# Optimization experiments

Hardware: AMD Instinct MI355X
Metric: run time of the kernel (lower is better)

The kernel has to match this reference:

```python
import jax, jax.numpy as jnp
import numpy as np

# ---- config (matches init_kwargs + VMamba/MambaIR SS2D defaults) ----
B, LEN, C, H, W = 2, 3, 64, 64, 64
N_STATE = 16           # d_state
D_INNER = 2 * C        # expand=2
DT_RANK = C // 16      # ceil(d_model/16)
K = 4                  # 4 scan directions
EPS = 1e-5


def _ln_last(x, g, b):
    m = x.mean(-1, keepdims=True)
    v = x.var(-1, keepdims=True)
    return (x - m) * jax.lax.rsqrt(v + EPS) * g + b


def _instance_ln(x):
    # kalman.utils.layer_norm: normalize each sample over (C,H,W), no affine
    m = x.mean(axis=(1, 2, 3), keepdims=True)
    v = x.var(axis=(1, 2, 3), keepdims=True)
    return (x - m) * jax.lax.rsqrt(v + EPS)


def _gn(x, g, b):
    # GroupNorm with num_groups=1 on NCHW
    m = x.mean(axis=(1, 2, 3), keepdims=True)
    v = x.var(axis=(1, 2, 3), keepdims=True)
    return (x - m) * jax.lax.rsqrt(v + EPS) * g[None, :, None, None] + b[None, :, None, None]


def _conv2d(x, w, b, groups=1):
    y = jax.lax.conv_general_dilated(x, w, (1, 1), 'SAME',
            dimension_numbers=('NCHW', 'OIHW', 'NCHW'), feature_group_count=groups)
    return y + b[None, :, None, None]


def _selective_scan(xs, dts, Bs, Cs, A, Ds, dt_bias):
    # xs, dts: (Bt,K,D,L); Bs, Cs: (Bt,K,N,L); A: (K,D,N); Ds, dt_bias: (K,D)
    delta = jax.nn.softplus(dts + dt_bias[None, :, :, None])
    u_t = jnp.moveaxis(xs, -1, 0)      # (L,Bt,K,D)
    d_t = jnp.moveaxis(delta, -1, 0)
    B_t = jnp.moveaxis(Bs, -1, 0)      # (L,Bt,K,N)
    C_t = jnp.moveaxis(Cs, -1, 0)
    h0 = jnp.zeros((xs.shape[0], K, xs.shape[2], A.shape[-1]), xs.dtype)

    def step(h, inp):
        u, d, Bv, Cv = inp
        dA = jnp.exp(d[..., None] * A)                                  # (Bt,K,D,N)
        h = dA * h + d[..., None] * Bv[:, :, None, :] * u[..., None]
        y = jnp.einsum('bkdn,bkn->bkd', h, Cv)
        return h, y

    _, ys = jax.lax.scan(step, h0, (u_t, d_t, B_t, C_t))
    ys = jnp.moveaxis(ys, 0, -1)                                        # (Bt,K,D,L)
    return ys + xs * Ds[None, :, :, None]


def _ss2d(x, in_proj_w, dwconv_w, dwconv_b, x_proj_w, dt_proj_w, dt_proj_b,
          A_logs, Ds, out_norm_g, out_norm_b, out_proj_w):
    Bt, Hh, Ww, Cc = x.shape
    L = Hh * Ww
    xz = x @ in_proj_w.T                               # (Bt,H,W,2*Di)
    xx, z = jnp.split(xz, 2, axis=-1)
    xx = jnp.transpose(xx, (0, 3, 1, 2))               # (Bt,Di,H,W)
    xx = jax.nn.silu(_conv2d(xx, dwconv_w, dwconv_b, groups=D_INNER))
    hw = xx.reshape(Bt, D_INNER, L)
    wh = jnp.transpose(xx, (0, 1, 3, 2)).reshape(Bt, D_INNER, L)
    xs = jnp.stack([hw, wh, hw[..., ::-1], wh[..., ::-1]], axis=1)      # (Bt,4,Di,L)
    x_dbl = jnp.einsum('bkdl,kcd->bkcl', xs, x_proj_w)
    dts = jnp.einsum('bkrl,kdr->bkdl', x_dbl[:, :, :DT_RANK], dt_proj_w)
    Bs = x_dbl[:, :, DT_RANK:DT_RANK + N_STATE]
    Cs = x_dbl[:, :, DT_RANK + N_STATE:]
    A = -jnp.exp(A_logs)                               # (K,Di,N)
    out_y = _selective_scan(xs, dts, Bs, Cs, A, Ds, dt_proj_b)
    inv = out_y[:, 2:4, :, ::-1]

    def wh2hw(y):
        return jnp.transpose(y.reshape(Bt, D_INNER, Ww, Hh), (0, 1, 3, 2)).reshape(Bt, D_INNER, L)

    y = out_y[:, 0] + inv[:, 0] + wh2hw(out_y[:, 1]) + wh2hw(inv[:, 1])
    y = jnp.transpose(y.reshape(Bt, D_INNER, Hh, Ww), (0, 2, 3, 1))
    y = _ln_last(y, out_norm_g, out_norm_b)
    y = y * jax.nn.silu(z)
    return y @ out_proj_w.T


def setup_inputs() -> dict:
    key = jax.random.key(0)
    ks = jax.random.split(key, 16)
    rn = lambda k, s, sc=0.05: jax.random.normal(k, s, jnp.float32) * sc
    inp = {}
    inp['image_sequence'] = jax.random.normal(ks[0], (B, LEN, C, H, W), jnp.float32)
    inp['difficult_zone'] = jax.random.normal(ks[1], (B, C, H, W), jnp.float32)
    inp['sigma'] = jax.random.uniform(ks[2], (B, C, H, W), jnp.float32)
    inp['gn1_g'] = jnp.ones((3 * C,)); inp['gn1_b'] = jnp.zeros((3 * C,))
    inp['conv1_w'] = rn(ks[3], (C, 3 * C, 3, 3)); inp['conv1_b'] = jnp.zeros((C,))
    inp['gn2_g'] = jnp.ones((C,)); inp['gn2_b'] = jnp.zeros((C,))
    inp['conv2_w'] = rn(ks[4], (C, C, 3, 3)); inp['conv2_b'] = jnp.zeros((C,))
    inp['skip_w'] = rn(ks[5], (C, 3 * C, 1, 1)); inp['skip_b'] = jnp.zeros((C,))
    inp['ln1_g'] = jnp.ones((C,)); inp['ln1_b'] = jnp.zeros((C,))
    inp['ln2_g'] = jnp.ones((C,)); inp['ln2_b'] = jnp.zeros((C,))
    inp['in_proj_w'] = rn(ks[6], (2 * D_INNER, C))
    inp['dwconv_w'] = rn(ks[7], (D_INNER, 1, 3, 3)); inp['dwconv_b'] = jnp.zeros((D_INNER,))
    inp['x_proj_w'] = rn(ks[8], (K, DT_RANK + 2 * N_STATE, D_INNER))
    inp['dt_proj_w'] = rn(ks[9], (K, D_INNER, DT_RANK), 0.2)
    inp['dt_proj_b'] = rn(ks[10], (K, D_INNER), 0.1)
    inp['A_logs'] = jnp.log(jnp.broadcast_to(jnp.arange(1, N_STATE + 1, dtype=jnp.float32), (K, D_INNER, N_STATE)))
    inp['Ds'] = jnp.ones((K, D_INNER))
    inp['out_norm_g'] = jnp.ones((D_INNER,)); inp['out_norm_b'] = jnp.zeros((D_INNER,))
    inp['out_proj_w'] = rn(ks[11], (C, D_INNER))
    inp['fc1_w'] = rn(ks[12], (C, C)); inp['fc1_b'] = jnp.zeros((C,))
    inp['fc2_w'] = rn(ks[13], (C, C)); inp['fc2_b'] = jnp.zeros((C,))
    return inp


def reference(image_sequence, difficult_zone, sigma,
              gn1_g, gn1_b, conv1_w, conv1_b, gn2_g, gn2_b, conv2_w, conv2_b, skip_w, skip_b,
              ln1_g, ln1_b, ln2_g, ln2_b,
              in_proj_w, dwconv_w, dwconv_b, x_proj_w, dt_proj_w, dt_proj_b,
              A_logs, Ds, out_norm_g, out_norm_b, out_proj_w,
              fc1_w, fc1_b, fc2_w, fc2_b):
    Bsz, Lf, Cc, Hh, Ww = image_sequence.shape
    # per-frame layer_norm; frames are independent so fold them into batch
    img = _instance_ln(image_sequence.reshape(Bsz * Lf, Cc, Hh, Ww)).reshape(Bsz, Lf, Cc, Hh, Ww)
    dz = jnp.broadcast_to(difficult_zone[:, None], (Bsz, Lf, Cc, Hh, Ww))
    sg = jnp.broadcast_to(sigma[:, None], (Bsz, Lf, Cc, Hh, Ww))
    x = jnp.concatenate([dz, img, sg], axis=2).reshape(Bsz * Lf, 3 * Cc, Hh, Ww)
    # ConvolutionalResBlock (GN -> SiLU -> conv, x2, + 1x1 skip)
    h = _conv2d(jax.nn.silu(_gn(x, gn1_g, gn1_b)), conv1_w, conv1_b)
    h = _conv2d(jax.nn.silu(_gn(h, gn2_g, gn2_b)), conv2_w, conv2_b)
    x = h + _conv2d(x, skip_w, skip_b)
    # VSSBlock (pre-norm): x + SS2D(LN(x)); x + Mlp(LN(x))
    x = jnp.transpose(x, (0, 2, 3, 1))                 # NHWC
    x = x + _ss2d(_ln_last(x, ln1_g, ln1_b), in_proj_w, dwconv_w, dwconv_b,
                  x_proj_w, dt_proj_w, dt_proj_b, A_logs, Ds,
                  out_norm_g, out_norm_b, out_proj_w)
    xm = _ln_last(x, ln2_g, ln2_b)
    x = x + (jax.nn.gelu(xm @ fc1_w.T + fc1_b) @ fc2_w.T + fc2_b)
    x = jnp.transpose(x, (0, 3, 1, 2)).reshape(Bsz, Lf, Cc, Hh, Ww)
    return x
```

## Files before the change

kernel.cpp:

```cpp
#include <hip/hip_runtime.h>
#include <hip/hip_bf16.h>

typedef unsigned short ushortT;
typedef short short8v __attribute__((ext_vector_type(8)));
typedef float float4v __attribute__((ext_vector_type(4)));

#define NBL 6
#define NC 64
#define NC3 192
#define NHW 4096
#define NDI 128
#define NNS 16
#define NDR 4
#define NK 4
#define NL 4096
#define NCH 128
#define SCLEN 32
#define NSTATE 49152

static const size_t F_XCAT  = 0;
static const size_t F_ACT1  = 4718592;
static const size_t F_H1    = 9437184;
static const size_t F_ACT2  = 11010048;
static const size_t F_H2    = 12582912;
static const size_t F_XRES  = 14155776;
static const size_t F_XXIN  = 15728640;
static const size_t F_Z     = 18874368;
static const size_t F_XXC   = 22020096;
static const size_t F_XDBL  = 25165824;
static const size_t F_YS    = 28704768;
static const size_t F_X1    = 44433408;
static const size_t F_X2    = 46006272;
static const size_t F_STATS = 47579136;
static const size_t F_TOTAL = 47579184;

__device__ __forceinline__ float wred64(float v) {
#pragma unroll
  for (int m = 32; m; m >>= 1) v += __shfl_xor(v, m, 64);
  return v;
}

__device__ __forceinline__ float silu(float v) {
  return v / (1.f + __expf(-v));
}

__device__ __forceinline__ ushortT f2bf(float f) {
  unsigned int u = __builtin_bit_cast(unsigned int, f);
  unsigned int r = (u + 0x7FFFu + ((u >> 16) & 1u)) >> 16;
  return (ushortT)r;
}

__device__ __forceinline__ float bf2f(ushortT u) {
  return __builtin_bit_cast(float, (unsigned int)u << 16);
}

__device__ __forceinline__ int map_pos(int k, int l) {
  if (k == 0) return l;
  if (k == 1) return ((l & 63) << 6) | (l >> 6);
  if (k == 2) return 4095 - l;
  int lp = 4095 - l;
  return ((lp & 63) << 6) | (lp >> 6);
}

__device__ __forceinline__ float softplus_fast(float a) {
  float t = exp2f(a * 1.44269504f);
  float r = 0.69314718f * __log2f(1.f + t);
  return (a > 20.f) ? a : r;
}

__device__ __forceinline__ void pow_tree(float E1, float4v& e0, float4v& e1,
                                         float4v& e2, float4v& e3) {
  float E2 = E1 * E1, E3 = E2 * E1, E4 = E2 * E2;
  float E5 = E4 * E1, E6 = E4 * E2, E7 = E4 * E3, E8 = E4 * E4;
  e0[0] = E1; e0[1] = E2; e0[2] = E3; e0[3] = E4;
  e1[0] = E5; e1[1] = E6; e1[2] = E7; e1[3] = E8;
  e2[0] = E8 * E1; e2[1] = E8 * E2; e2[2] = E8 * E3; e2[3] = E8 * E4;
  e3[0] = E8 * E5; e3[1] = E8 * E6; e3[2] = E8 * E7; e3[3] = E8 * E8;
}

__global__ __launch_bounds__(256) void wtrans_kernel(const float* __restrict__ src,
                                                     float* __restrict__ dst, int O, int C) {
  int id = blockIdx.x * 256 + threadIdx.x;
  if (id >= O * C) return;
  int c = id / O, o = id % O;
  dst[id] = src[o * C + c];
}

__global__ __launch_bounds__(256) void stats1_kernel(const float* __restrict__ in, int n,
                                                     double* __restrict__ part) {
  int bi = blockIdx.x;
  int s = bi >> 5, j = bi & 31;
  int slice = n >> 5;
  const float4* p = (const float4*)(in + (size_t)s * n + (size_t)j * slice);
  int n4 = slice >> 2;
  double dsum = 0.0, dsq = 0.0;
  for (int i = threadIdx.x; i < n4; i += 256) {
    float4 v = p[i];
    dsum += (double)((v.x + v.y) + (v.z + v.w));
    dsq += (double)v.x * v.x + (double)v.y * v.y + (double)v.z * v.z + (double)v.w * v.w;
  }
  __shared__ double s1[256], s2[256];
  s1[threadIdx.x] = dsum; s2[threadIdx.x] = dsq;
  __syncthreads();
  for (int off = 128; off; off >>= 1) {
    if (threadIdx.x < off) { s1[threadIdx.x] += s1[threadIdx.x + off]; s2[threadIdx.x] += s2[threadIdx.x + off]; }
    __syncthreads();
  }
  if (threadIdx.x == 0) { part[2 * bi] = s1[0]; part[2 * bi + 1] = s2[0]; }
}

__global__ __launch_bounds__(64) void stats2_kernel(const double* __restrict__ part, int n,
                                                    float* __restrict__ mean_out,
                                                    float* __restrict__ rstd_out) {
  int s = blockIdx.x;
  int lane = threadIdx.x;
  double sum = 0.0, sq = 0.0;
  if (lane < 32) { sum = part[2 * (s * 32 + lane)]; sq = part[2 * (s * 32 + lane) + 1]; }
#pragma unroll
  for (int m = 16; m; m >>= 1) { sum += __shfl_xor(sum, m, 64); sq += __shfl_xor(sq, m, 64); }
  if (lane == 0) {
    double mean = sum / n;
    double var = sq / n - mean * mean;
    mean_out[s] = (float)mean;
    rstd_out[s] = (float)(1.0 / sqrt(var + 1e-5));
  }
}

__global__ __launch_bounds__(256) void build_xcat_kernel(const float* __restrict__ img,
                                                         const float* __restrict__ dz,
                                                         const float* __restrict__ sg,
                                                         const float* __restrict__ stats,
                                                         float* __restrict__ xcat) {
  size_t gid = (size_t)blockIdx.x * 256 + threadIdx.x;
  int p = gid & 4095;
  size_t r = gid >> 12;
  int ch = (int)(r % NC3);
  int bl = (int)(r / NC3);
  int b = bl / 3;
  float v;
  if (ch < 64) {
    v = dz[((size_t)b * NC + ch) * NHW + p];
  } else if (ch < 128) {
    float m = stats[bl], rs = stats[8 + bl];
    v = (img[((size_t)bl * NC + (ch - 64)) * NHW + p] - m) * rs;
  } else {
    v = sg[((size_t)b * NC + (ch - 128)) * NHW + p];
  }
  xcat[gid] = v;
}

template <int CCH>
__global__ __launch_bounds__(256) void gnsilu_t_kernel(const float* __restrict__ in,
                                                       const float* __restrict__ g,
                                                       const float* __restrict__ b,
                                                       const float* __restrict__ stats,
                                                       ushortT* __restrict__ outb) {
  int bi = blockIdx.x;
  int bl = bi >> 6, h = bi & 63;
  __shared__ ushortT tile[CCH][66];
  float m = stats[bl], rs = stats[8 + bl];
  int t = threadIdx.x;
  for (int idx = t; idx < CCH * 64; idx += 256) {
    int ch = idx >> 6, w = idx & 63;
    float v = in[(((size_t)bl * CCH + ch) << 12) + (h << 6) + w];
    v = (v - m) * rs * g[ch] + b[ch];
    v = silu(v);
    tile[ch][w] = f2bf(v);
  }
  __syncthreads();
  constexpr int C8 = CCH / 8;
  for (int idx = t; idx < 64 * C8; idx += 256) {
    int w = idx / C8, c8 = idx % C8;
    short8v v;
#pragma unroll
    for (int j = 0; j < 8; ++j) v[j] = (short)tile[c8 * 8 + j][w];
    *(short8v*)&outb[(size_t)(bl * 4096 + h * 64 + w) * CCH + c8 * 8] = v;
  }
}

__global__ __launch_bounds__(256) void wprep_kernel(const float* __restrict__ w,
                                                    ushortT* __restrict__ out,
                                                    int CIN, int KT) {
  int id = blockIdx.x * 256 + threadIdx.x;
  int j = id & 7;
  int lane = (id >> 3) & 63;
  int nt = (id >> 9) & 3;
  int rest = id >> 11;
  int kt = rest % KT;
  int tap = rest / KT;
  int oc = nt * 16 + (lane & 15);
  int ic = kt * 32 + ((lane >> 4) << 3) + j;
  int r = tap / 3, s = tap % 3;
  out[id] = f2bf(w[(((size_t)oc * CIN + ic) * 3 + r) * 3 + s]);
}

template <int CIN>
__global__ __launch_bounds__(256) void conv_mfma_kernel(const ushortT* __restrict__ actb,
                                                        const ushortT* __restrict__ wb,
                                                        const float* __restrict__ bias,
                                                        float* __restrict__ out) {
  constexpr int KT = CIN / 32;
  constexpr int STRIDE = CIN + 8;
  constexpr int C8 = CIN / 8;
  int bi = blockIdx.x;
  int nh = bi & 1;
  int h = (bi >> 1) & 63;
  int bl = bi >> 7;
  int t = threadIdx.x;
  int wv = t >> 6, lane = t & 63;
  __shared__ ushortT lds[66 * STRIDE];
  float4v acc0 = {0.f, 0.f, 0.f, 0.f};
  float4v acc1 = {0.f, 0.f, 0.f, 0.f};
  int lrow = lane & 15;
  int lk = (lane >> 4) << 3;
  for (int dy = 0; dy < 3; ++dy) {
    int hh = h + dy - 1;
    bool valid = (hh >= 0) && (hh < 64);
    int hc = valid ? hh : 0;
    if (dy) __syncthreads();
    const ushortT* src = actb + (size_t)(bl * 4096 + hc * 64) * CIN;
    for (int idx = t; idx < 64 * C8; idx += 256) {
      int w = idx / C8, c8 = idx % C8;
      short8v v = {0, 0, 0, 0, 0, 0, 0, 0};
      if (valid) v = *(const short8v*)&src[(size_t)w * CIN + c8 * 8];
      *(short8v*)&lds[(w + 1) * STRIDE + c8 * 8] = v;
    }
    if (t < 2 * C8) {
      int which = t / C8, c8 = t % C8;
      short8v z = {0, 0, 0, 0, 0, 0, 0, 0};
      *(short8v*)&lds[(which ? 65 : 0) * STRIDE + c8 * 8] = z;
    }
    __syncthreads();
    for (int dx = 0; dx < 3; ++dx) {
      int tap = dy * 3 + dx;
      int wl = (wv << 4) + lrow + dx;
#pragma unroll
      for (int kt = 0; kt < KT; ++kt) {
        short8v a = *(const short8v*)&lds[wl * STRIDE + kt * 32 + lk];
        const ushortT* wp = wb + ((size_t)(((tap * KT + kt) * 4 + (nh << 1)) * 64 + lane) << 3);
        short8v b0 = *(const short8v*)&wp[0];
        short8v b1 = *(const short8v*)&wp[512];
        acc0 = __builtin_amdgcn_mfma_f32_16x16x32_bf16(a, b0, acc0, 0, 0, 0);
        acc1 = __builtin_amdgcn_mfma_f32_16x16x32_bf16(a, b1, acc1, 0, 0, 0);
      }
    }
  }
  int oc0 = (nh << 5) + lrow;
  int oc1 = oc0 + 16;
  int w0 = (wv << 4) + ((lane >> 4) << 2);
  float bv0 = bias[oc0], bv1 = bias[oc1];
  float4 o0 = make_float4(acc0[0] + bv0, acc0[1] + bv0, acc0[2] + bv0, acc0[3] + bv0);
  float4 o1 = make_float4(acc1[0] + bv1, acc1[1] + bv1, acc1[2] + bv1, acc1[3] + bv1);
  *(float4*)&out[(((size_t)bl * 64 + oc0) << 12) + (h << 6) + w0] = o0;
  *(float4*)&out[(((size_t)bl * 64 + oc1) << 12) + (h << 6) + w0] = o1;
}

__global__ __launch_bounds__(256) void skip_kernel(const float* __restrict__ xcat,
                                                   const float* __restrict__ h2,
                                                   const float* __restrict__ skwt,
                                                   const float* __restrict__ skb,
                                                   float* __restrict__ xres) {
  int bi = blockIdx.x;
  int bl = bi >> 6, h = bi & 63;
  int t = threadIdx.x;
  int oc = t & 63, w0 = (t >> 6) << 4;
  __shared__ float lds[64][64];
  float acc[16];
#pragma unroll
  for (int i = 0; i < 16; ++i) acc[i] = 0.f;
  for (int cc = 0; cc < 3; ++cc) {
    __syncthreads();
    for (int idx = t; idx < 4096; idx += 256) {
      int ch = idx >> 6, w = idx & 63;
      lds[ch][w] = xcat[(((size_t)bl * NC3 + cc * 64 + ch) << 12) + (h << 6) + w];
    }
    __syncthreads();
    for (int ch = 0; ch < 64; ++ch) {
      float wv = skwt[((cc << 6) + ch) * 64 + oc];
#pragma unroll
      for (int i = 0; i < 16; ++i) acc[i] += wv * lds[ch][w0 + i];
    }
  }
  float bv = skb[oc];
  int p0 = (h << 6) + w0;
#pragma unroll
  for (int i = 0; i < 16; ++i) {
    float hv = h2[(((size_t)bl * 64 + oc) << 12) + p0 + i];
    xres[((size_t)bl * NHW + p0 + i) * 64 + oc] = acc[i] + bv + hv;
  }
}

__global__ __launch_bounds__(256) void inproj_kernel(const float* __restrict__ xres,
                                                     const float* __restrict__ g,
                                                     const float* __restrict__ b,
                                                     const float* __restrict__ wt,
                                                     float* __restrict__ xxin,
                                                     float* __restrict__ z) {
  int wv = threadIdx.x >> 6, lane = threadIdx.x & 63;
  size_t pi0 = (size_t)blockIdx.x << 4;
  __shared__ float xb[64][16];
  float gv = g[lane], bv = b[lane];
#pragma unroll
  for (int j = 0; j < 4; ++j) {
    int p = (wv << 2) + j;
    float x = xres[(pi0 + p) * 64 + lane];
    float s = wred64(x);
    float s2 = wred64(x * x);
    float m = s * (1.f / 64), var = s2 * (1.f / 64) - m * m;
    float rstd = rsqrtf(var + 1e-5f);
    xb[lane][p] = (x - m) * rstd * gv + bv;
  }
  __syncthreads();
  int oc = (wv << 6) + lane;
  float4v a0 = {0.f, 0.f, 0.f, 0.f}, a1 = a0, a2 = a0, a3 = a0;
  for (int c = 0; c < 64; ++c) {
    float w = wt[(c << 8) + oc];
    const float4v* xr = (const float4v*)&xb[c][0];
    a0 += w * xr[0];
    a1 += w * xr[1];
    a2 += w * xr[2];
    a3 += w * xr[3];
  }
  float acc[16];
  *(float4v*)&acc[0] = a0;
  *(float4v*)&acc[4] = a1;
  *(float4v*)&acc[8] = a2;
  *(float4v*)&acc[12] = a3;
  float* dst = (oc < 128) ? xxin : z;
  int oco = (oc < 128) ? oc : (oc - 128);
#pragma unroll
  for (int p = 0; p < 16; ++p) dst[((pi0 + p) << 7) + oco] = acc[p];
}

__global__ __launch_bounds__(256) void dwconv_kernel(const float* __restrict__ xx,
                                                     const float* __restrict__ w,
                                                     const float* __restrict__ b,
                                                     float* __restrict__ out) {
  size_t gid = (size_t)blockIdx.x * 256 + threadIdx.x;
  int d = gid & 127;
  size_t pi = gid >> 7;
  int p = (int)(pi & 4095);
  int bl = (int)(pi >> 12);
  int h = p >> 6, wq = p & 63;
  float acc = b[d];
  const float* wr = w + d * 9;
#pragma unroll
  for (int dy = -1; dy <= 1; ++dy) {
    int hh = h + dy;
    if (hh < 0 || hh >= 64) continue;
#pragma unroll
    for (int dx = -1; dx <= 1; ++dx) {
      int ww = wq + dx;
      if (ww < 0 || ww >= 64) continue;
      acc += wr[(dy + 1) * 3 + (dx + 1)] * xx[(((size_t)bl << 12) + (hh << 6) + ww) * 128 + d];
    }
  }
  out[pi * 128 + d] = silu(acc);
}

__global__ __launch_bounds__(256) void xdbl_kernel(const float* __restrict__ xxc,
                                                   const float* __restrict__ xpw,
                                                   float* __restrict__ xdbl) {
  int bi = blockIdx.x;
  int lt = bi & 63;
  int korder = (bi >> 6) & 1;
  int bl = bi >> 7;
  int lbase = lt << 6;
  __shared__ float xs[64 * 128];
  int t = threadIdx.x;
#pragma unroll
  for (int it = 0; it < 8; ++it) {
    int idx = it * 256 + t;
    int i = idx >> 5, d4 = idx & 31;
    int l = lbase + i;
    int pos = korder ? (((l & 63) << 6) | (l >> 6)) : l;
    float4 v = *(const float4*)&xxc[((size_t)bl * NHW + pos) * 128 + (d4 << 2)];
    int slot = d4 ^ (i & 7);
    *(float4*)&xs[i * 128 + (slot << 2)] = v;
  }
  __syncthreads();
  int wv = __builtin_amdgcn_readfirstlane(t >> 6);
  int lane = t & 63;
  int k_w = korder + ((wv >= 2) ? 2 : 0);
  int c0 = (wv & 1) * 18;
  float acc[18];
#pragma unroll
  for (int j = 0; j < 18; ++j) acc[j] = 0.f;
  const float* wbase = xpw + (size_t)(k_w * 36 + c0) * 128;
  for (int d4 = 0; d4 < 32; ++d4) {
    int slot = d4 ^ (lane & 7);
    float4 x4 = *(const float4*)&xs[lane * 128 + (slot << 2)];
#pragma unroll
    for (int j = 0; j < 18; ++j) {
      float4 w4 = *(const float4*)&wbase[j * 128 + (d4 << 2)];
      acc[j] += w4.x * x4.x + w4.y * x4.y + w4.z * x4.z + w4.w * x4.w;
    }
  }
  int lout = (k_w < 2) ? (lbase + lane) : (4095 - lbase - lane);
  size_t obase = ((size_t)(bl * 4 + k_w) * 36 + c0) * (size_t)NL + lout;
#pragma unroll
  for (int j = 0; j < 18; ++j)
    xdbl[obase + (size_t)j * NL] = acc[j];
}

__global__ __launch_bounds__(128) void scan_pass1_kernel(const float* __restrict__ xdbl,
                                                         const float* __restrict__ xxc,
                                                         const float* __restrict__ dtw,
                                                         const float* __restrict__ dtb,
                                                         const float* __restrict__ Alog,
                                                         float* __restrict__ chunkSdt,
                                                         ushortT* __restrict__ chunkH16) {
  int bi = blockIdx.x;
  int chunk = bi & (NCH - 1);
  int bk = bi >> 7;
  int k = bk & 3, bl = bk >> 2;
  int d = threadIdx.x;
  float4 wv = *(const float4*)(dtw + (size_t)(((k << 7) + d) << 2));
  float bias = dtb[(k << 7) + d];
  const float* ar = Alog + (size_t)(((k << 7) + d) << 4);
  float a1v = -__expf(ar[0]) * 1.44269504f;
  bool geom = true;
#pragma unroll
  for (int n = 1; n < 16; ++n) {
    float an = -__expf(ar[n]) * 1.44269504f;
    geom = geom && (fabsf(an - (float)(n + 1) * a1v) <= 1e-3f * fabsf((float)(n + 1) * a1v) + 1e-6f);
  }
  __shared__ float xd[SCLEN][20];
  int l0 = chunk << 5;
  for (int idx = threadIdx.x; idx < 20 * SCLEN; idx += 128) {
    int c = idx >> 5, li = idx & 31;
    xd[li][c] = xdbl[((size_t)bk * 36 + c) * (size_t)NL + l0 + li];
  }
  __syncthreads();
  const float* uB = xxc + ((size_t)bl << 19) + d;
  float4v h0 = {0.f, 0.f, 0.f, 0.f}, h1 = h0, h2 = h0, h3 = h0;
  float sdt = 0.f;
  float u_nxt = uB[(size_t)map_pos(k, l0) << 7];
  if (geom) {
    for (int li = 0; li < SCLEN; ++li) {
      float u = u_nxt;
      int nl = (li < SCLEN - 1) ? (li + 1) : (SCLEN - 1);
      u_nxt = uB[(size_t)map_pos(k, l0 + nl) << 7];
      const float4v* row = (const float4v*)&xd[li][0];
      float4v q0 = row[0];
      float accq = bias + wv.x * q0[0] + wv.y * q0[1] + wv.z * q0[2] + wv.w * q0[3];
      float dt = softplus_fast(accq);
      float dtu = dt * u;
      sdt += dt;
      float4v b0 = row[1], b1 = row[2], b2 = row[3], b3 = row[4];
      float4v e0, e1, e2, e3;
      pow_tree(exp2f(a1v * dt), e0, e1, e2, e3);
      h0 = e0 * h0 + dtu * b0;
      h1 = e1 * h1 + dtu * b1;
      h2 = e2 * h2 + dtu * b2;
      h3 = e3 * h3 + dtu * b3;
    }
  } else {
    float4v a0v, a1q, a2q, a3q;
#pragma unroll
    for (int j = 0; j < 4; ++j) {
      a0v[j] = -__expf(ar[j]) * 1.44269504f;
      a1q[j] = -__expf(ar[4 + j]) * 1.44269504f;
      a2q[j] = -__expf(ar[8 + j]) * 1.44269504f;
      a3q[j] = -__expf(ar[12 + j]) * 1.44269504f;
    }
    for (int li = 0; li < SCLEN; ++li) {
      float u = u_nxt;
      int nl = (li < SCLEN - 1) ? (li + 1) : (SCLEN - 1);
      u_nxt = uB[(size_t)map_pos(k, l0 + nl) << 7];
      const float4v* row = (const float4v*)&xd[li][0];
      float4v q0 = row[0];
      float accq = bias + wv.x * q0[0] + wv.y * q0[1] + wv.z * q0[2] + wv.w * q0[3];
      float dt = softplus_fast(accq);
      float dtu = dt * u;
      sdt += dt;
      float4v b0 = row[1], b1 = row[2], b2 = row[3], b3 = row[4];
      float4v e0, e1, e2, e3;
#pragma unroll
      for (int j = 0; j < 4; ++j) {
        e0[j] = exp2f(a0v[j] * dt);
        e1[j] = exp2f(a1q[j] * dt);
        e2[j] = exp2f(a2q[j] * dt);
        e3[j] = exp2f(a3q[j] * dt);
      }
      h0 = e0 * h0 + dtu * b0;
      h1 = e1 * h1 + dtu * b1;
      h2 = e2 * h2 + dtu * b2;
      h3 = e3 * h3 + dtu * b3;
    }
  }
  size_t base = (size_t)chunk * NSTATE + (((size_t)bk << 7) + (size_t)d) * 16;
  chunkSdt[(size_t)chunk * 3072 + (bk << 7) + d] = sdt;
  short8v s0, s1;
#pragma unroll
  for (int j = 0; j < 4; ++j) {
    s0[j] = (short)f2bf(h0[j]);
    s0[4 + j] = (short)f2bf(h1[j]);
    s1[j] = (short)f2bf(h2[j]);
    s1[4 + j] = (short)f2bf(h3[j]);
  }
  *(short8v*)&chunkH16[base + 0] = s0;
  *(short8v*)&chunkH16[base + 8] = s1;
}

__global__ __launch_bounds__(256) void scan_pass2_kernel(const float* __restrict__ chunkSdt,
                                                         const ushortT* __restrict__ chunkH16,
                                                         const float* __restrict__ Alog,
                                                         ushortT* __restrict__ chunkHS16) {
  size_t state = (size_t)blockIdx.x * 256 + threadIdx.x;
  float an = -__expf(Alog[state & 8191]) * 1.44269504f;
  int kd = (int)(state >> 4);
  float h = 0.f;
  for (int j = 0; j < NCH; ++j) {
    size_t idx = (size_t)j * NSTATE + state;
    chunkHS16[idx] = f2bf(h);
    float sdt = chunkSdt[(size_t)j * 3072 + kd];
    h = exp2f(an * sdt) * h + bf2f(chunkH16[idx]);
  }
}

__global__ __launch_bounds__(128) void scan_pass3_kernel(const float* __restrict__ xdbl,
                                                         const float* __restrict__ xxc,
                                                         const float* __restrict__ dtw,
                                                         const float* __restrict__ dtb,
                                                         const float* __restrict__ Alog,
                                                         const ushortT* __restrict__ chunkHS16,
                                                         ushortT* __restrict__ ys16) {
  int bi = blockIdx.x;
  int chunk = bi & (NCH - 1);
  int bk = bi >> 7;
  int k = bk & 3, bl = bk >> 2;
  int d = threadIdx.x;
  float4 wv = *(const float4*)(dtw + (size_t)(((k << 7) + d) << 2));
  float bias = dtb[(k << 7) + d];
  const float* ar = Alog + (size_t)(((k << 7) + d) << 4);
  float a1v = -__expf(ar[0]) * 1.44269504f;
  bool geom = true;
#pragma unroll
  for (int n = 1; n < 16; ++n) {
    float an = -__expf(ar[n]) * 1.44269504f;
    geom = geom && (fabsf(an - (float)(n + 1) * a1v) <= 1e-3f * fabsf((float)(n + 1) * a1v) + 1e-6f);
  }
  __shared__ float xd[SCLEN][36];
  int l0 = chunk << 5;
  for (int idx = threadIdx.x; idx < 36 * SCLEN; idx += 128) {
    int c = idx >> 5, li = idx & 31;
    xd[li][c] = xdbl[((size_t)bk * 36 + c) * (size_t)NL + l0 + li];
  }
  __syncthreads();
  const float* uB = xxc + ((size_t)bl << 19) + d;
  ushortT* yB = ys16 + ((size_t)bk << 19) + d;
  size_t base = (size_t)chunk * NSTATE + (((size_t)bk << 7) + (size_t)d) * 16;
  float4v h0, h1, h2, h3;
  {
    short8v s0 = *(const short8v*)&chunkHS16[base + 0];
    short8v s1 = *(const short8v*)&chunkHS16[base + 8];
#pragma unroll
    for (int j = 0; j < 4; ++j) {
      h0[j] = bf2f((ushortT)s0[j]);
      h1[j] = bf2f((ushortT)s0[4 + j]);
      h2[j] = bf2f((ushortT)s1[j]);
      h3[j] = bf2f((ushortT)s1[4 + j]);
    }
  }
  float u_nxt = uB[(size_t)map_pos(k, l0) << 7];
  if (geom) {
    for (int li = 0; li < SCLEN; ++li) {
      float u = u_nxt;
      int nl = (li < SCLEN - 1) ? (li + 1) : (SCLEN - 1);
      u_nxt = uB[(size_t)map_pos(k, l0 + nl) << 7];
      const float4v* row = (const float4v*)&xd[li][0];
      float4v q0 = row[0];
      float accq = bias + wv.x * q0[0] + wv.y * q0[1] + wv.z * q0[2] + wv.w * q0[3];
      float dt = softplus_fast(accq);
      float dtu = dt * u;
      float4v b0 = row[1], b1 = row[2], b2 = row[3], b3 = row[4];
      float4v c0 = row[5], c1 = row[6], c2 = row[7], c3 = row[8];
      float4v e0, e1, e2, e3;
      pow_tree(exp2f(a1v * dt), e0, e1, e2, e3);
      h0 = e0 * h0 + dtu * b0;
      h1 = e1 * h1 + dtu * b1;
      h2 = e2 * h2 + dtu * b2;
      h3 = e3 * h3 + dtu * b3;
      float4v sy = h0 * c0;
      sy += h1 * c1;
      sy += h2 * c2;
      sy += h3 * c3;
      yB[(size_t)(l0 + li) << 7] = f2bf((sy[0] + sy[1]) + (sy[2] + sy[3]));
    }
  } else {
    float4v a0v, a1q, a2q, a3q;
#pragma unroll
    for (int j = 0; j < 4; ++j) {
      a0v[j] = -__expf(ar[j]) * 1.44269504f;
      a1q[j] = -__expf(ar[4 + j]) * 1.44269504f;
      a2q[j] = -__expf(ar[8 + j]) * 1.44269504f;
      a3q[j] = -__expf(ar[12 + j]) * 1.44269504f;
    }
    for (int li = 0; li < SCLEN; ++li) {
      float u = u_nxt;
      int nl = (li < SCLEN - 1) ? (li + 1) : (SCLEN - 1);
      u_nxt = uB[(size_t)map_pos(k, l0 + nl) << 7];
      const float4v* row = (const float4v*)&xd[li][0];
      float4v q0 = row[0];
      float accq = bias + wv.x * q0[0] + wv.y * q0[1] + wv.z * q0[2] + wv.w * q0[3];
      float dt = softplus_fast(accq);
      float dtu = dt * u;
      float4v b0 = row[1], b1 = row[2], b2 = row[3], b3 = row[4];
      float4v c0 = row[5], c1 = row[6], c2 = row[7], c3 = row[8];
      float4v e0, e1, e2, e3;
#pragma unroll
      for (int j = 0; j < 4; ++j) {
        e0[j] = exp2f(a0v[j] * dt);
        e1[j] = exp2f(a1q[j] * dt);
        e2[j] = exp2f(a2q[j] * dt);
        e3[j] = exp2f(a3q[j] * dt);
      }
      h0 = e0 * h0 + dtu * b0;
      h1 = e1 * h1 + dtu * b1;
      h2 = e2 * h2 + dtu * b2;
      h3 = e3 * h3 + dtu * b3;
      float4v sy = h0 * c0;
      sy += h1 * c1;
      sy += h2 * c2;
      sy += h3 * c3;
      yB[(size_t)(l0 + li) << 7] = f2bf((sy[0] + sy[1]) + (sy[2] + sy[3]));
    }
  }
}

__global__ __launch_bounds__(256) void outproj_kernel(const ushortT* __restrict__ ys16,
                                                      const float* __restrict__ xxc,
                                                      const float* __restrict__ Ds,
                                                      const float* __restrict__ z,
                                                      const float* __restrict__ ong,
                                                      const float* __restrict__ onb,
                                                      const float* __restrict__ opwt,
                                                      const float* __restrict__ xres,
                                                      float* __restrict__ x1) {
  int wv = threadIdx.x >> 6, lane = threadIdx.x & 63;
  size_t pi0 = (size_t)blockIdx.x << 4;
  __shared__ float gb[128][16];
  float og0 = ong[lane], ob0 = onb[lane];
  float og1 = ong[64 + lane], ob1 = onb[64 + lane];
  float ds0 = Ds[lane] + Ds[128 + lane] + Ds[256 + lane] + Ds[384 + lane];
  float ds1 = Ds[64 + lane] + Ds[192 + lane] + Ds[320 + lane] + Ds[448 + lane];
#pragma unroll
  for (int j = 0; j < 4; ++j) {
    int p = (wv << 2) + j;
    size_t pp = pi0 + p;
    int bl = (int)(pp >> 12);
    int pg = (int)(pp & 4095);
    int h = pg >> 6, w = pg & 63;
    int l1 = (w << 6) | h;
    size_t base = ((size_t)bl * 4) << 12;
    size_t i0 = (base + pg) << 7;
    size_t i1 = (base + 4096 + l1) << 7;
    size_t i2 = (base + 2 * 4096 + (4095 - pg)) << 7;
    size_t i3 = (base + 3 * 4096 + (4095 - l1)) << 7;
    float xx0 = xxc[(pp << 7) + lane], xx1 = xxc[(pp << 7) + 64 + lane];
    float y0 = bf2f(ys16[i0 + lane]) + bf2f(ys16[i1 + lane]) + bf2f(ys16[i2 + lane]) +
               bf2f(ys16[i3 + lane]) + xx0 * ds0;
    float y1 = bf2f(ys16[i0 + 64 + lane]) + bf2f(ys16[i1 + 64 + lane]) +
               bf2f(ys16[i2 + 64 + lane]) + bf2f(ys16[i3 + 64 + lane]) + xx1 * ds1;
    float s = wred64(y0 + y1);
    float s2 = wred64(y0 * y0 + y1 * y1);
    float m = s * (1.f / 128), var = s2 * (1.f / 128) - m * m;
    float rstd = rsqrtf(var + 1e-5f);
    float z0 = z[(pp << 7) + lane], z1 = z[(pp << 7) + 64 + lane];
    gb[lane][p] = ((y0 - m) * rstd * og0 + ob0) * silu(z0);
    gb[64 + lane][p] = ((y1 - m) * rstd * og1 + ob1) * silu(z1);
  }
  __syncthreads();
  int p0 = wv << 2;
  float4v acc = {0.f, 0.f, 0.f, 0.f};
  for (int c = 0; c < 128; ++c) {
    float w = opwt[(c << 6) + lane];
    acc += w * (*(const float4v*)&gb[c][p0]);
  }
  float accs[4];
  *(float4v*)&accs[0] = acc;
#pragma unroll
  for (int j = 0; j < 4; ++j) {
    size_t pp = pi0 + p0 + j;
    x1[pp * 64 + lane] = xres[pp * 64 + lane] + accs[j];
  }
}

__global__ __launch_bounds__(256) void mlp_kernel(const float* __restrict__ x1,
                                                  const float* __restrict__ g2,
                                                  const float* __restrict__ b2,
                                                  const float* __restrict__ w1t,
                                                  const float* __restrict__ bb1,
                                                  const float* __restrict__ w2t,
                                                  const float* __restrict__ bb2,
                                                  float* __restrict__ out) {
  int wv = threadIdx.x >> 6, lane = threadIdx.x & 63;
  size_t pi0 = (size_t)blockIdx.x << 4;
  __shared__ float xb[64][16], tb[64][16];
  __shared__ float ot[64][17];
  float gv = g2[lane], bv = b2[lane];
  float xsave[4];
#pragma unroll
  for (int j = 0; j < 4; ++j) {
    int p = (wv << 2) + j;
    float xv = x1[(pi0 + p) * 64 + lane];
    xsave[j] = xv;
    float s = wred64(xv), s2 = wred64(xv * xv);
    float m = s * (1.f / 64), var = s2 * (1.f / 64) - m * m;
    float rstd = rsqrtf(var + 1e-5f);
    xb[lane][p] = (xv - m) * rstd * gv + bv;
  }
  __syncthreads();
  int p0 = wv << 2;
  float bb1v = bb1[lane];
  float4v acc = {bb1v, bb1v, bb1v, bb1v};
  for (int c = 0; c < 64; ++c) {
    float w = w1t[(c << 6) + lane];
    acc += w * (*(const float4v*)&xb[c][p0]);
  }
  float us[4];
  *(float4v*)&us[0] = acc;
#pragma unroll
  for (int j = 0; j < 4; ++j) {
    float u = us[j];
    float tt = tanhf(0.7978845608028654f * (u + 0.044715f * u * u * u));
    tb[lane][p0 + j] = 0.5f * u * (1.f + tt);
  }
  __syncthreads();
  float bb2v = bb2[lane];
  float4v acc2 = {bb2v, bb2v, bb2v, bb2v};
  for (int c = 0; c < 64; ++c) {
    float w = w2t[(c << 6) + lane];
    acc2 += w * (*(const float4v*)&tb[c][p0]);
  }
  float o2[4];
  *(float4v*)&o2[0] = acc2;
#pragma unroll
  for (int j = 0; j < 4; ++j)
    ot[lane][p0 + j] = xsave[j] + o2[j];
  __syncthreads();
  int bl = (int)(pi0 >> 12);
  int pg0 = (int)(pi0 & 4095);
  int t = threadIdx.x;
  int c = t >> 2, q = t & 3;
  float4 v = make_float4(ot[c][(q << 2) + 0], ot[c][(q << 2) + 1],
                         ot[c][(q << 2) + 2], ot[c][(q << 2) + 3]);
  *(float4*)&out[(((size_t)bl * 64 + c) << 12) + pg0 + (q << 2)] = v;
}

extern "C" void kernel_launch(void* const* d_in, const int* in_sizes, int n_in,
                              void* d_out, int out_size, void* d_ws, size_t ws_size,
                              hipStream_t stream) {
  const float* img  = (const float*)d_in[0];
  const float* dz   = (const float*)d_in[1];
  const float* sg   = (const float*)d_in[2];
  const float* gn1g = (const float*)d_in[3];
  const float* gn1b = (const float*)d_in[4];
  const float* c1w  = (const float*)d_in[5];
  const float* c1b  = (const float*)d_in[6];
  const float* gn2g = (const float*)d_in[7];
  const float* gn2b = (const float*)d_in[8];
  const float* c2w  = (const float*)d_in[9];
  const float* c2b  = (const float*)d_in[10];
  const float* skw  = (const float*)d_in[11];
  const float* skb  = (const float*)d_in[12];
  const float* ln1g = (const float*)d_in[13];
  const float* ln1b = (const float*)d_in[14];
  const float* ln2g = (const float*)d_in[15];
  const float* ln2b = (const float*)d_in[16];
  const float* ipw  = (const float*)d_in[17];
  const float* dww  = (const float*)d_in[18];
  const float* dwb  = (const float*)d_in[19];
  const float* xpw  = (const float*)d_in[20];
  const float* dtw  = (const float*)d_in[21];
  const float* dtb  = (const float*)d_in[22];
  const float* Alog = (const float*)d_in[23];
  const float* Dsp  = (const float*)d_in[24];
  const float* ong  = (const float*)d_in[25];
  const float* onb  = (const float*)d_in[26];
  const float* opw  = (const float*)d_in[27];
  const float* f1w  = (const float*)d_in[28];
  const float* f1b  = (const float*)d_in[29];
  const float* f2w  = (const float*)d_in[30];
  const float* f2b  = (const float*)d_in[31];

  float* out = (float*)d_out;
  float* ws = (float*)d_ws;
  if (ws_size < F_TOTAL * sizeof(float)) return;

  float* xcat  = ws + F_XCAT;
  float* h1    = ws + F_H1;
  float* h2    = ws + F_H2;
  float* xres  = ws + F_XRES;
  float* xxin  = ws + F_XXIN;
  float* zbuf  = ws + F_Z;
  float* xxc   = ws + F_XXC;
  float* xdbl  = ws + F_XDBL;
  float* x1    = ws + F_X1;
  float* stats = ws + F_STATS;
  ushortT* act1b = (ushortT*)(ws + F_ACT1);
  ushortT* act2b = (ushortT*)(ws + F_ACT2);
  double* part  = (double*)(ws + F_X2);
  ushortT* wb1  = (ushortT*)(ws + F_X2 + 1024);
  ushortT* wb2  = wb1 + 110592;
  ushortT* ys16     = (ushortT*)(ws + F_YS);
  ushortT* chunkH16 = (ushortT*)(ws + F_YS + 6291456);
  float*   chunkSdt = ws + F_YS + 6291456 + 3145728;
  ushortT* chunkHS16 = (ushortT*)(ws + F_XCAT);
  float* wt_sk = ws + F_ACT1;
  float* wt_ip = ws + F_XCAT;
  float* wt_op = ws + F_XXIN;
  float* wt_f1 = ws + F_XXIN + 8192;
  float* wt_f2 = ws + F_XXIN + 12288;

  wprep_kernel<<<432, 256, 0, stream>>>(c1w, wb1, NC3, 6);
  wprep_kernel<<<144, 256, 0, stream>>>(c2w, wb2, NC, 2);
  stats1_kernel<<<NBL * 32, 256, 0, stream>>>(img, NC * NHW, part);
  stats2_kernel<<<NBL, 64, 0, stream>>>(part, NC * NHW, stats + 0, stats + 8);
  build_xcat_kernel<<<18432, 256, 0, stream>>>(img, dz, sg, stats, xcat);
  stats1_kernel<<<NBL * 32, 256, 0, stream>>>(xcat, NC3 * NHW, part);
  stats2_kernel<<<NBL, 64, 0, stream>>>(part, NC3 * NHW, stats + 16, stats + 24);
  gnsilu_t_kernel<NC3><<<NBL * 64, 256, 0, stream>>>(xcat, gn1g, gn1b, stats + 16, act1b);
  conv_mfma_kernel<NC3><<<NBL * 64 * 2, 256, 0, stream>>>(act1b, wb1, c1b, h1);
  wtrans_kernel<<<48, 256, 0, stream>>>(skw, wt_sk, 64, 192);
  stats1_kernel<<<NBL * 32, 256, 0, stream>>>(h1, NC * NHW, part);
  stats2_kernel<<<NBL, 64, 0, stream>>>(part, NC * NHW, stats + 32, stats + 40);
  gnsilu_t_kernel<NC><<<NBL * 64, 256, 0, stream>>>(h1, gn2g, gn2b, stats + 32, act2b);
  conv_mfma_kernel<NC><<<NBL * 64 * 2, 256, 0, stream>>>(act2b, wb2, c2b, h2);
  skip_kernel<<<NBL * 64, 256, 0, stream>>>(xcat, h2, wt_sk, skb, xres);
  wtrans_kernel<<<64, 256, 0, stream>>>(ipw, wt_ip, 256, 64);
  inproj_kernel<<<1536, 256, 0, stream>>>(xres, ln1g, ln1b, wt_ip, xxin, zbuf);
  dwconv_kernel<<<12288, 256, 0, stream>>>(xxin, dww, dwb, xxc);
  wtrans_kernel<<<32, 256, 0, stream>>>(opw, wt_op, 64, 128);
  wtrans_kernel<<<16, 256, 0, stream>>>(f1w, wt_f1, 64, 64);
  wtrans_kernel<<<16, 256, 0, stream>>>(f2w, wt_f2, 64, 64);
  xdbl_kernel<<<NBL * 2 * 64, 256, 0, stream>>>(xxc, xpw, xdbl);
  scan_pass1_kernel<<<24 * NCH, 128, 0, stream>>>(xdbl, xxc, dtw, dtb, Alog, chunkSdt, chunkH16);
  scan_pass2_kernel<<<192, 256, 0, stream>>>(chunkSdt, chunkH16, Alog, chunkHS16);
  scan_pass3_kernel<<<24 * NCH, 128, 0, stream>>>(xdbl, xxc, dtw, dtb, Alog, chunkHS16, ys16);
  outproj_kernel<<<1536, 256, 0, stream>>>(ys16, xxc, Dsp, zbuf, ong, onb, wt_op, xres, x1);
  mlp_kernel<<<1536, 256, 0, stream>>>(x1, ln2g, ln2b, wt_f1, f1b, wt_f2, f2b, out);
}
```

Before: 343.9 us.

## Eliminate xcat buffer by computing GN1 stats analytically and fusing concat into consumers

Folds all weight transposes and conv weight prep into one prep kernel. Computes the GroupNorm statistics of the concatenated input analytically from per-source sums, using the instance-normalized image's known variance, so the concatenated tensor is never materialized. The GN+SiLU and skip kernels now read dz/img/sg directly. This removes a large write and re-read of xcat plus several launches. It also adds unroll pragmas in the scan loops and pads a shared-memory tile.

```diff
diff --git a/kernel.cpp b/kernel.cpp
--- a/kernel.cpp
+++ b/kernel.cpp
@@ -17,6 +17,7 @@
 #define NCH 128
 #define SCLEN 32
 #define NSTATE 49152
+#define NSAMP 262144
 
 static const size_t F_XCAT  = 0;
 static const size_t F_ACT1  = 4718592;
@@ -29,6 +30,7 @@
 static const size_t F_XXC   = 22020096;
 static const size_t F_XDBL  = 25165824;
 static const size_t F_YS    = 28704768;
+static const size_t F_WTS   = 41287680;
 static const size_t F_X1    = 44433408;
 static const size_t F_X2    = 46006272;
 static const size_t F_STATS = 47579136;
@@ -78,12 +80,89 @@
   e3[0] = E8 * E5; e3[1] = E8 * E6; e3[2] = E8 * E7; e3[3] = E8 * E8;
 }
 
-__global__ __launch_bounds__(256) void wtrans_kernel(const float* __restrict__ src,
-                                                     float* __restrict__ dst, int O, int C) {
-  int id = blockIdx.x * 256 + threadIdx.x;
-  if (id >= O * C) return;
-  int c = id / O, o = id % O;
-  dst[id] = src[o * C + c];
+__global__ __launch_bounds__(256) void prep_kernel(const float* __restrict__ skw,
+                                                   const float* __restrict__ ipw,
+                                                   const float* __restrict__ opw,
+                                                   const float* __restrict__ f1w,
+                                                   const float* __restrict__ f2w,
+                                                   const float* __restrict__ c1w,
+                                                   const float* __restrict__ c2w,
+                                                   float* __restrict__ wt_sk,
+                                                   float* __restrict__ wt_ip,
+                                                   float* __restrict__ wt_op,
+                                                   float* __restrict__ wt_f1,
+                                                   float* __restrict__ wt_f2,
+                                                   ushortT* __restrict__ wb1,
+                                                   ushortT* __restrict__ wb2) {
+  int bi = blockIdx.x;
+  int t = threadIdx.x;
+  if (bi < 48) {
+    int id = bi * 256 + t;
+    int c = id / 64, o = id % 64;
+    wt_sk[id] = skw[o * 192 + c];
+  } else if (bi < 112) {
+    int id = (bi - 48) * 256 + t;
+    int c = id / 256, o = id % 256;
+    wt_ip[id] = ipw[o * 64 + c];
+  } else if (bi < 144) {
+    int id = (bi - 112) * 256 + t;
+    int c = id / 64, o = id % 64;
+    wt_op[id] = opw[o * 128 + c];
+  } else if (bi < 160) {
+    int id = (bi - 144) * 256 + t;
+    int c = id / 64, o = id % 64;
+    wt_f1[id] = f1w[o * 64 + c];
+  } else if (bi < 176) {
+    int id = (bi - 160) * 256 + t;
+    int c = id / 64, o = id % 64;
+    wt_f2[id] = f2w[o * 64 + c];
+  } else if (bi < 608) {
+    int id = (bi - 176) * 256 + t;
+    int j = id & 7, lane = (id >> 3) & 63, nt = (id >> 9) & 3;
+    int rest = id >> 11;
+    int kt = rest % 6, tap = rest / 6;
+    int oc = nt * 16 + (lane & 15);
+    int ic = kt * 32 + ((lane >> 4) << 3) + j;
+    int r = tap / 3, s = tap % 3;
+    wb1[id] = f2bf(c1w[(((size_t)oc * 192 + ic) * 3 + r) * 3 + s]);
+  } else {
+    int id = (bi - 608) * 256 + t;
+    int j = id & 7, lane = (id >> 3) & 63, nt = (id >> 9) & 3;
+    int rest = id >> 11;
+    int kt = rest % 2, tap = rest / 2;
+    int oc = nt * 16 + (lane & 15);
+    int ic = kt * 32 + ((lane >> 4) << 3) + j;
+    int r = tap / 3, s = tap % 3;
+    wb2[id] = f2bf(c2w[(((size_t)oc * 64 + ic) * 3 + r) * 3 + s]);
+  }
+}
+
+__global__ __launch_bounds__(256) void stats1_all_kernel(const float* __restrict__ img,
+                                                         const float* __restrict__ dz,
+                                                         const float* __restrict__ sg,
+                                                         double* __restrict__ part) {
+  int bi = blockIdx.x;
+  int s = bi >> 5, j = bi & 31;
+  const float* srcb = (s < 6) ? (img + (size_t)s * NSAMP)
+                   : (s < 8) ? (dz + (size_t)(s - 6) * NSAMP)
+                             : (sg + (size_t)(s - 8) * NSAMP);
+  int slice = NSAMP >> 5;
+  const float4* p = (const float4*)(srcb + (size_t)j * slice);
+  int n4 = slice >> 2;
+  double dsum = 0.0, dsq = 0.0;
+  for (int i = threadIdx.x; i < n4; i += 256) {
+    float4 v = p[i];
+    dsum += (double)((v.x + v.y) + (v.z + v.w));
+    dsq += (double)v.x * v.x + (double)v.y * v.y + (double)v.z * v.z + (double)v.w * v.w;
+  }
+  __shared__ double s1[256], s2[256];
+  s1[threadIdx.x] = dsum; s2[threadIdx.x] = dsq;
+  __syncthreads();
+  for (int off = 128; off; off >>= 1) {
+    if (threadIdx.x < off) { s1[threadIdx.x] += s1[threadIdx.x + off]; s2[threadIdx.x] += s2[threadIdx.x + off]; }
+    __syncthreads();
+  }
+  if (threadIdx.x == 0) { part[2 * bi] = s1[0]; part[2 * bi + 1] = s2[0]; }
 }
 
 __global__ __launch_bounds__(256) void stats1_kernel(const float* __restrict__ in, int n,
@@ -126,30 +205,81 @@
   }
 }
 
-__global__ __launch_bounds__(256) void build_xcat_kernel(const float* __restrict__ img,
+__global__ __launch_bounds__(64) void stats2_comb_kernel(const double* __restrict__ part,
+                                                         float* __restrict__ stats) {
+  int s = blockIdx.x;
+  int lane = threadIdx.x;
+  if (s < 6) {
+    double sum = 0.0, sq = 0.0;
+    if (lane < 32) { sum = part[2 * (s * 32 + lane)]; sq = part[2 * (s * 32 + lane) + 1]; }
+#pragma unroll
+    for (int m = 16; m; m >>= 1) { sum += __shfl_xor(sum, m, 64); sq += __shfl_xor(sq, m, 64); }
+    if (lane == 0) {
+      double mean = sum / NSAMP;
+      double var = sq / NSAMP - mean * mean;
+      stats[s] = (float)mean;
+      stats[8 + s] = (float)(1.0 / sqrt(var + 1e-5));
+    }
+    return;
+  }
+  if (lane == 0) {
+    double sums[10], sqs[10];
+    for (int q = 0; q < 10; ++q) {
+      double a = 0.0, b2 = 0.0;
+      for (int j = 0; j < 32; ++j) { a += part[2 * (q * 32 + j)]; b2 += part[2 * (q * 32 + j) + 1]; }
+      sums[q] = a; sqs[q] = b2;
+    }
+    const double N = (double)NSAMP;
+    for (int bl = 0; bl < 6; ++bl) {
+      int b = bl / 3;
+      double mi = sums[bl] / N;
+      double vi = sqs[bl] / N - mi * mi;
+      double ssq_norm = N * (vi / (vi + 1e-5));
+      double sum_cat = sums[6 + b] + sums[8 + b];
+      double ssq_cat = sqs[6 + b] + ssq_norm + sqs[8 + b];
+      double mean = sum_cat / (3.0 * N);
+      double var = ssq_cat / (3.0 * N) - mean * mean;
+      stats[16 + bl] = (float)mean;
+      stats[24 + bl] = (float)(1.0 / sqrt(var + 1e-5));
+    }
+  }
+}
+
+__global__ __launch_bounds__(256) void gnsilu_cat_kernel(const float* __restrict__ img,
                                                          const float* __restrict__ dz,
                                                          const float* __restrict__ sg,
+                                                         const float* __restrict__ g,
+                                                         const float* __restrict__ b,
                                                          const float* __restrict__ stats,
-                                                         float* __restrict__ xcat) {
-  size_t gid = (size_t)blockIdx.x * 256 + threadIdx.x;
-  int p = gid & 4095;
-  size_t r = gid >> 12;
-  int ch = (int)(r % NC3);
-  int bl = (int)(r / NC3);
-  int b = bl / 3;
-  float v;
-  if (ch < 64) {
-    v = dz[((size_t)b * NC + ch) * NHW + p];
-  } else if (ch < 128) {
-    float m = stats[bl], rs = stats[8 + bl];
-    v = (img[((size_t)bl * NC + (ch - 64)) * NHW + p] - m) * rs;
-  } else {
-    v = sg[((size_t)b * NC + (ch - 128)) * NHW + p];
-  }
-  xcat[gid] = v;
-}
-
-template <int CCH>
+                                                         ushortT* __restrict__ outb) {
+  int bi = blockIdx.x;
+  int bl = bi >> 6, h = bi & 63;
+  int bb = bl / 3;
+  __shared__ ushortT tile[NC3][66];
+  float mi = stats[bl], rsi = stats[8 + bl];
+  float mc = stats[16 + bl], rsc = stats[24 + bl];
+  int t = threadIdx.x;
+  for (int idx = t; idx < NC3 * 64; idx += 256) {
+    int ch = idx >> 6, w = idx & 63;
+    int hw = (h << 6) + w;
+    float v;
+    if (ch < 64) v = dz[((size_t)bb * NC + ch) * NHW + hw];
+    else if (ch < 128) v = (img[((size_t)bl * NC + (ch - 64)) * NHW + hw] - mi) * rsi;
+    else v = sg[((size_t)bb * NC + (ch - 128)) * NHW + hw];
+    v = (v - mc) * rsc * g[ch] + b[ch];
+    tile[ch][w] = f2bf(silu(v));
+  }
+  __syncthreads();
+  constexpr int C8 = NC3 / 8;
+  for (int idx = t; idx < 64 * C8; idx += 256) {
+    int w = idx / C8, c8 = idx % C8;
+    short8v v;
+#pragma unroll
+    for (int j = 0; j < 8; ++j) v[j] = (short)tile[c8 * 8 + j][w];
+    *(short8v*)&outb[(size_t)(bl * 4096 + h * 64 + w) * NC3 + c8 * 8] = v;
+  }
+}
+
 __global__ __launch_bounds__(256) void gnsilu_t_kernel(const float* __restrict__ in,
                                                        const float* __restrict__ g,
                                                        const float* __restrict__ b,
@@ -157,41 +287,24 @@
                                                        ushortT* __restrict__ outb) {
   int bi = blockIdx.x;
   int bl = bi >> 6, h = bi & 63;
-  __shared__ ushortT tile[CCH][66];
+  __shared__ ushortT tile[NC][66];
   float m = stats[bl], rs = stats[8 + bl];
   int t = threadIdx.x;
-  for (int idx = t; idx < CCH * 64; idx += 256) {
+  for (int idx = t; idx < NC * 64; idx += 256) {
     int ch = idx >> 6, w = idx & 63;
-    float v = in[(((size_t)bl * CCH + ch) << 12) + (h << 6) + w];
+    float v = in[(((size_t)bl * NC + ch) << 12) + (h << 6) + w];
     v = (v - m) * rs * g[ch] + b[ch];
-    v = silu(v);
-    tile[ch][w] = f2bf(v);
-  }
-  __syncthreads();
-  constexpr int C8 = CCH / 8;
+    tile[ch][w] = f2bf(silu(v));
+  }
+  __syncthreads();
+  constexpr int C8 = NC / 8;
   for (int idx = t; idx < 64 * C8; idx += 256) {
     int w = idx / C8, c8 = idx % C8;
     short8v v;
 #pragma unroll
     for (int j = 0; j < 8; ++j) v[j] = (short)tile[c8 * 8 + j][w];
-    *(short8v*)&outb[(size_t)(bl * 4096 + h * 64 + w) * CCH + c8 * 8] = v;
-  }
-}
-
-__global__ __launch_bounds__(256) void wprep_kernel(const float* __restrict__ w,
-                                                    ushortT* __restrict__ out,
-                                                    int CIN, int KT) {
-  int id = blockIdx.x * 256 + threadIdx.x;
-  int j = id & 7;
-  int lane = (id >> 3) & 63;
-  int nt = (id >> 9) & 3;
-  int rest = id >> 11;
-  int kt = rest % KT;
-  int tap = rest / KT;
-  int oc = nt * 16 + (lane & 15);
-  int ic = kt * 32 + ((lane >> 4) << 3) + j;
-  int r = tap / 3, s = tap % 3;
-  out[id] = f2bf(w[(((size_t)oc * CIN + ic) * 3 + r) * 3 + s]);
+    *(short8v*)&outb[(size_t)(bl * 4096 + h * 64 + w) * NC + c8 * 8] = v;
+  }
 }
 
 template <int CIN>
@@ -255,15 +368,20 @@
   *(float4*)&out[(((size_t)bl * 64 + oc1) << 12) + (h << 6) + w0] = o1;
 }
 
-__global__ __launch_bounds__(256) void skip_kernel(const float* __restrict__ xcat,
+__global__ __launch_bounds__(256) void skip_kernel(const float* __restrict__ img,
+                                                   const float* __restrict__ dz,
+                                                   const float* __restrict__ sg,
+                                                   const float* __restrict__ stats,
                                                    const float* __restrict__ h2,
                                                    const float* __restrict__ skwt,
                                                    const float* __restrict__ skb,
                                                    float* __restrict__ xres) {
   int bi = blockIdx.x;
   int bl = bi >> 6, h = bi & 63;
+  int bb = bl / 3;
   int t = threadIdx.x;
   int oc = t & 63, w0 = (t >> 6) << 4;
+  float mi = stats[bl], rsi = stats[8 + bl];
   __shared__ float lds[64][64];
   float acc[16];
 #pragma unroll
@@ -272,7 +390,12 @@
     __syncthreads();
     for (int idx = t; idx < 4096; idx += 256) {
       int ch = idx >> 6, w = idx & 63;
-      lds[ch][w] = xcat[(((size_t)bl * NC3 + cc * 64 + ch) << 12) + (h << 6) + w];
+      int hw = (h << 6) + w;
+      float v;
+      if (cc == 0) v = dz[((size_t)bb * NC + ch) * NHW + hw];
+      else if (cc == 1) v = (img[((size_t)bl * NC + ch) * NHW + hw] - mi) * rsi;
+      else v = sg[((size_t)bb * NC + ch) * NHW + hw];
+      lds[ch][w] = v;
     }
     __syncthreads();
     for (int ch = 0; ch < 64; ++ch) {
@@ -437,6 +560,7 @@
   float sdt = 0.f;
   float u_nxt = uB[(size_t)map_pos(k, l0) << 7];
   if (geom) {
+#pragma unroll 2
     for (int li = 0; li < SCLEN; ++li) {
       float u = u_nxt;
       int nl = (li < SCLEN - 1) ? (li + 1) : (SCLEN - 1);
@@ -541,7 +665,7 @@
     float an = -__expf(ar[n]) * 1.44269504f;
     geom = geom && (fabsf(an - (float)(n + 1) * a1v) <= 1e-3f * fabsf((float)(n + 1) * a1v) + 1e-6f);
   }
-  __shared__ float xd[SCLEN][36];
+  __shared__ float xd[SCLEN][40];
   int l0 = chunk << 5;
   for (int idx = threadIdx.x; idx < 36 * SCLEN; idx += 128) {
     int c = idx >> 5, li = idx & 31;
@@ -565,6 +689,7 @@
   }
   float u_nxt = uB[(size_t)map_pos(k, l0) << 7];
   if (geom) {
+#pragma unroll 2
     for (int li = 0; li < SCLEN; ++li) {
       float u = u_nxt;
       int nl = (li < SCLEN - 1) ? (li + 1) : (SCLEN - 1);
@@ -789,7 +914,6 @@
   float* ws = (float*)d_ws;
   if (ws_size < F_TOTAL * sizeof(float)) return;
 
-  float* xcat  = ws + F_XCAT;
   float* h1    = ws + F_H1;
   float* h2    = ws + F_H2;
   float* xres  = ws + F_XRES;
@@ -802,39 +926,31 @@
   ushortT* act1b = (ushortT*)(ws + F_ACT1);
   ushortT* act2b = (ushortT*)(ws + F_ACT2);
   double* part  = (double*)(ws + F_X2);
-  ushortT* wb1  = (ushortT*)(ws + F_X2 + 1024);
-  ushortT* wb2  = wb1 + 110592;
+  float* wt_sk = ws + F_WTS;
+  float* wt_ip = ws + F_WTS + 16384;
+  float* wt_op = ws + F_WTS + 32768;
+  float* wt_f1 = ws + F_WTS + 40960;
+  float* wt_f2 = ws + F_WTS + 45056;
+  ushortT* wb1 = (ushortT*)(ws + F_WTS + 49152);
+  ushortT* wb2 = wb1 + 110592;
   ushortT* ys16     = (ushortT*)(ws + F_YS);
   ushortT* chunkH16 = (ushortT*)(ws + F_YS + 6291456);
   float*   chunkSdt = ws + F_YS + 6291456 + 3145728;
   ushortT* chunkHS16 = (ushortT*)(ws + F_XCAT);
-  float* wt_sk = ws + F_ACT1;
-  float* wt_ip = ws + F_XCAT;
-  float* wt_op = ws + F_XXIN;
-  float* wt_f1 = ws + F_XXIN + 8192;
-  float* wt_f2 = ws + F_XXIN + 12288;
-
-  wprep_kernel<<<432, 256, 0, stream>>>(c1w, wb1, NC3, 6);
-  wprep_kernel<<<144, 256, 0, stream>>>(c2w, wb2, NC, 2);
-  stats1_kernel<<<NBL * 32, 256, 0, stream>>>(img, NC * NHW, part);
-  stats2_kernel<<<NBL, 64, 0, stream>>>(part, NC * NHW, stats + 0, stats + 8);
-  build_xcat_kernel<<<18432, 256, 0, stream>>>(img, dz, sg, stats, xcat);
-  stats1_kernel<<<NBL * 32, 256, 0, stream>>>(xcat, NC3 * NHW, part);
-  stats2_kernel<<<NBL, 64, 0, stream>>>(part, NC3 * NHW, stats + 16, stats + 24);
-  gnsilu_t_kernel<NC3><<<NBL * 64, 256, 0, stream>>>(xcat, gn1g, gn1b, stats + 16, act1b);
+
+  prep_kernel<<<752, 256, 0, stream>>>(skw, ipw, opw, f1w, f2w, c1w, c2w,
+                                       wt_sk, wt_ip, wt_op, wt_f1, wt_f2, wb1, wb2);
+  stats1_all_kernel<<<320, 256, 0, stream>>>(img, dz, sg, part);
+  stats2_comb_kernel<<<7, 64, 0, stream>>>(part, stats);
+  gnsilu_cat_kernel<<<NBL * 64, 256, 0, stream>>>(img, dz, sg, gn1g, gn1b, stats, act1b);
   conv_mfma_kernel<NC3><<<NBL * 64 * 2, 256, 0, stream>>>(act1b, wb1, c1b, h1);
-  wtrans_kernel<<<48, 256, 0, stream>>>(skw, wt_sk, 64, 192);
   stats1_kernel<<<NBL * 32, 256, 0, stream>>>(h1, NC * NHW, part);
   stats2_kernel<<<NBL, 64, 0, stream>>>(part, NC * NHW, stats + 32, stats + 40);
-  gnsilu_t_kernel<NC><<<NBL * 64, 256, 0, stream>>>(h1, gn2g, gn2b, stats + 32, act2b);
+  gnsilu_t_kernel<<<NBL * 64, 256, 0, stream>>>(h1, gn2g, gn2b, stats + 32, act2b);
   conv_mfma_kernel<NC><<<NBL * 64 * 2, 256, 0, stream>>>(act2b, wb2, c2b, h2);
-  skip_kernel<<<NBL * 64, 256, 0, stream>>>(xcat, h2, wt_sk, skb, xres);
-  wtrans_kernel<<<64, 256, 0, stream>>>(ipw, wt_ip, 256, 64);
+  skip_kernel<<<NBL * 64, 256, 0, stream>>>(img, dz, sg, stats, h2, wt_sk, skb, xres);
   inproj_kernel<<<1536, 256, 0, stream>>>(xres, ln1g, ln1b, wt_ip, xxin, zbuf);
   dwconv_kernel<<<12288, 256, 0, stream>>>(xxin, dww, dwb, xxc);
-  wtrans_kernel<<<32, 256, 0, stream>>>(opw, wt_op, 64, 128);
-  wtrans_kernel<<<16, 256, 0, stream>>>(f1w, wt_f1, 64, 64);
-  wtrans_kernel<<<16, 256, 0, stream>>>(f2w, wt_f2, 64, 64);
   xdbl_kernel<<<NBL * 2 * 64, 256, 0, stream>>>(xxc, xpw, xdbl);
   scan_pass1_kernel<<<24 * NCH, 128, 0, stream>>>(xdbl, xxc, dtw, dtb, Alog, chunkSdt, chunkH16);
   scan_pass2_kernel<<<192, 256, 0, stream>>>(chunkSdt, chunkH16, Alog, chunkHS16);
```

Result: faster. 324.2 us (-5.7%).
